# Performance work log

Measured on AMD Instinct MI355X. Metric: run time of the kernel, lower is better.

The kernel has to match this reference:

```python
import jax, jax.numpy as jnp
import numpy as np

NUM_CONTROL_POINTS = 4
# Standard Catmull-Rom spline basis (rows map [1, t, t^2, t^3] monomials to control points)
CATMULL_ROM_BASIS = 0.5 * np.array(
    [[0.0, 2.0, 0.0, 0.0],
     [-1.0, 0.0, 1.0, 0.0],
     [2.0, -5.0, 4.0, -1.0],
     [-1.0, 3.0, -3.0, 1.0]], dtype=np.float32)

BATCH, IN_F, OUT_F = 1024, 512, 512


def setup_inputs() -> dict:
    key = jax.random.key(0)
    k1, k2, k3, k4 = jax.random.split(key, 4)
    inp = jax.random.normal(k1, (BATCH, IN_F), dtype=jnp.float32)
    # phase spans [0, 2*pi) so both spline segments (mask = phase < 1.5*pi) are exercised
    phase = jax.random.uniform(k2, (BATCH,), dtype=jnp.float32) * (2.0 * jnp.pi)
    bound = 1.0 / np.sqrt(IN_F)
    weights = jax.random.uniform(k3, (NUM_CONTROL_POINTS, OUT_F, IN_F), dtype=jnp.float32,
                                 minval=-bound, maxval=bound)
    biases = jax.random.uniform(k4, (NUM_CONTROL_POINTS, OUT_F), dtype=jnp.float32,
                                minval=-bound, maxval=bound)
    return {"input": inp, "phase": phase, "weights": weights, "biases": biases}


def _spline_coeffs(phase):
    # Faithful to the original (including its overwrite bug): tt = [1, t^2, t^3, 0]
    basis = jnp.asarray(CATMULL_ROM_BASIS, dtype=phase.dtype)
    t0 = phase / (1.5 * jnp.pi)
    t1 = (phase - 0.5 * jnp.pi) / (1.5 * jnp.pi)
    ones, zeros = jnp.ones_like(phase), jnp.zeros_like(phase)
    tt0 = jnp.stack([ones, t0 * t0, t0 ** 3, zeros], axis=1)  # (B,4)
    tt1 = jnp.stack([ones, t1 * t1, t1 ** 3, zeros], axis=1)  # (B,4)
    mask = (phase < 1.5 * jnp.pi)[:, None]
    # Selecting per-sample coefficients before the weight contraction is exactly
    # equivalent to where(mask, tt0@B@W, tt1@B@W) since the map is linear in tt.
    return jnp.where(mask, tt0 @ basis, tt1 @ basis)  # (B,4) control-point coeffs


def reference(input, phase, weights, biases):
    c = _spline_coeffs(phase)                       # (B,4)
    # Fused form: apply the 4 shared control-point linear layers, then blend,
    # avoiding the (B,out,in) per-sample weight tensor. Same math as
    # (tt@B@W).reshape(B,out,in) @ input[:,:,None] + b.
    y4 = jnp.einsum('bi,coi->bco', input, weights)  # (B,4,out)
    out = jnp.einsum('bc,bco->bo', c, y4) + c @ biases  # (B,out)
    return out
```

## Files before the change

kernel.cpp:

```cpp
#include <hip/hip_runtime.h>


#define BATCH 1024
#define IN_F  512
#define OUT_F 512

constexpr int BM = 32;
constexpr int BO = 32;
constexpr int BK = 32;
constexpr int KITERS = IN_F / BK;

typedef unsigned short u16;
typedef __bf16 bf16x8 __attribute__((ext_vector_type(8)));
typedef float  f32x4  __attribute__((ext_vector_type(4)));
typedef float  f32x8  __attribute__((ext_vector_type(8)));

__device__ __forceinline__ bf16x8 cvt8(f32x8 v) {
  bf16x8 r;
#pragma unroll
  for (int i = 0; i < 8; ++i) r[i] = (__bf16)v[i];
  return r;
}

__global__ __launch_bounds__(128)
void PhaseLinear_kernel(const float* __restrict__ inp, const float* __restrict__ ph,
                        const float* __restrict__ wts, const float* __restrict__ bia,
                        float* __restrict__ outp) {
  __shared__ float sCoef[BM][4];

  const int tid = threadIdx.x;
  const int wv  = tid >> 6;
  const int l   = tid & 63;
  const int o0  = blockIdx.x * BO;
  const int b0  = blockIdx.y * BM;

  if (tid < BM) {
    const float PI = 3.14159265358979323846f;
    float p  = ph[b0 + tid];
    float t  = (p < 1.5f * PI) ? (p / (1.5f * PI)) : ((p - 0.5f * PI) / (1.5f * PI));
    float t2 = t * t, t3 = t2 * t;
    sCoef[tid][0] = t3 - 0.5f * t2;
    sCoef[tid][1] = 1.0f - 2.5f * t3;
    sCoef[tid][2] = 0.5f * t2 + 2.0f * t3;
    sCoef[tid][3] = -0.5f * t3;
  }
  __syncthreads();

  const int n = l & 15;
  const int q = l >> 4;

  const float* pa0 = inp + (size_t)(b0 + n) * IN_F + q * 8;
  const float* pa1 = pa0 + (size_t)16 * IN_F;
  const float* pw[4];
#pragma unroll
  for (int c = 0; c < 4; ++c)
    pw[c] = wts + ((size_t)c * OUT_F + o0 + wv * 16 + n) * IN_F + q * 8;

  f32x4 acc[2][4];
#pragma unroll
  for (int m = 0; m < 2; ++m)
#pragma unroll
    for (int c = 0; c < 4; ++c) acc[m][c] = (f32x4){0.f, 0.f, 0.f, 0.f};

  f32x8 cur[6];
  cur[0] = *(const f32x8*)(pa0);
  cur[1] = *(const f32x8*)(pa1);
#pragma unroll
  for (int c = 0; c < 4; ++c) cur[2 + c] = *(const f32x8*)(pw[c]);

#pragma unroll
  for (int kk = 0; kk < KITERS; ++kk) {
    f32x8 nxt[6];
    if (kk + 1 < KITERS) {
      const int off = (kk + 1) * BK;
      nxt[0] = *(const f32x8*)(pa0 + off);
      nxt[1] = *(const f32x8*)(pa1 + off);
#pragma unroll
      for (int c = 0; c < 4; ++c) nxt[2 + c] = *(const f32x8*)(pw[c] + off);
    }
    bf16x8 a0 = cvt8(cur[0]);
    bf16x8 a1 = cvt8(cur[1]);
#pragma unroll
    for (int c = 0; c < 4; ++c) {
      bf16x8 wf = cvt8(cur[2 + c]);
      acc[0][c] = __builtin_amdgcn_mfma_f32_16x16x32_bf16(a0, wf, acc[0][c], 0, 0, 0);
      acc[1][c] = __builtin_amdgcn_mfma_f32_16x16x32_bf16(a1, wf, acc[1][c], 0, 0, 0);
    }
#pragma unroll
    for (int j = 0; j < 6; ++j) cur[j] = nxt[j];
  }

  const int o = o0 + wv * 16 + n;
  float bs[4];
#pragma unroll
  for (int c = 0; c < 4; ++c) bs[c] = bia[c * OUT_F + o];

#pragma unroll
  for (int mf = 0; mf < 2; ++mf) {
#pragma unroll
    for (int r = 0; r < 4; ++r) {
      const int bl = mf * 16 + q * 4 + r;
      float v = 0.f;
#pragma unroll
      for (int c = 0; c < 4; ++c)
        v += sCoef[bl][c] * (acc[mf][c][r] + bs[c]);
      outp[(size_t)(b0 + bl) * OUT_F + o] = v;
    }
  }
}

extern "C" void kernel_launch(void* const* d_in, const int* in_sizes, int n_in,
                              void* d_out, int out_size, void* d_ws, size_t ws_size,
                              hipStream_t stream) {
  const float* inp = (const float*)d_in[0];
  const float* ph  = (const float*)d_in[1];
  const float* wts = (const float*)d_in[2];
  const float* bia = (const float*)d_in[3];
  float* outp = (float*)d_out;

  dim3 grid(OUT_F / BO, BATCH / BM);
  PhaseLinear_kernel<<<grid, 128, 0, stream>>>(inp, ph, wts, bia, outp);
}
```

Baseline: 84.39 us.

## Pre-convert inputs and weights to bf16 in workspace, enlarge batch tile to 64

Adds a separate conversion kernel that writes bf16 copies of the input and all four weight matrices into the workspace. The GEMM kernel then loads bf16 fragments directly instead of loading fp32 and converting on every iteration, which halves the bytes per load. Each block now holds four waves covering 64 batch rows, and the k-loop is manually double-buffered two steps at a time. The cost is an extra launch and a full read and write pass over the weights and input on every call.

```diff
diff --git a/kernel.cpp b/kernel.cpp
--- a/kernel.cpp
+++ b/kernel.cpp
@@ -5,31 +5,48 @@
 #define IN_F  512
 #define OUT_F 512
 
-constexpr int BM = 32;
+constexpr int BM = 64;
 constexpr int BO = 32;
 constexpr int BK = 32;
 constexpr int KITERS = IN_F / BK;
 
+constexpr int A_VECS = BATCH * IN_F / 4;
+constexpr int W_VECS = 4 * OUT_F * IN_F / 4;
+constexpr int CVT_VECS = A_VECS + W_VECS;
+constexpr size_t WS_A = 0;
+constexpr size_t WS_W = (size_t)BATCH * IN_F;
+
 typedef unsigned short u16;
+typedef __bf16 bf16x4 __attribute__((ext_vector_type(4)));
 typedef __bf16 bf16x8 __attribute__((ext_vector_type(8)));
 typedef float  f32x4  __attribute__((ext_vector_type(4)));
-typedef float  f32x8  __attribute__((ext_vector_type(8)));
 
-__device__ __forceinline__ bf16x8 cvt8(f32x8 v) {
-  bf16x8 r;
+__global__ __launch_bounds__(256)
+void cvt_kernel(const float* __restrict__ inp, const float* __restrict__ wts,
+                __bf16* __restrict__ ws) {
+  int v = blockIdx.x * 256 + threadIdx.x;
+  if (v >= CVT_VECS) return;
+  const float* src; __bf16* dst;
+  if (v < A_VECS) { src = inp + (size_t)v * 4;            dst = ws + WS_A + (size_t)v * 4; }
+  else { int u = v - A_VECS; src = wts + (size_t)u * 4;   dst = ws + WS_W + (size_t)u * 4; }
+  f32x4 x = *(const f32x4*)src;
+  bf16x4 y;
 #pragma unroll
-  for (int i = 0; i < 8; ++i) r[i] = (__bf16)v[i];
-  return r;
+  for (int i = 0; i < 4; ++i) y[i] = (__bf16)x[i];
+  *(bf16x4*)dst = y;
 }
 
-__global__ __launch_bounds__(128)
-void PhaseLinear_kernel(const float* __restrict__ inp, const float* __restrict__ ph,
-                        const float* __restrict__ wts, const float* __restrict__ bia,
-                        float* __restrict__ outp) {
+struct Frag { bf16x8 a0, a1, w0, w1, w2, w3; };
+
+__global__ __launch_bounds__(256)
+void PhaseLinear_kernel(const __bf16* __restrict__ ws, const float* __restrict__ ph,
+                        const float* __restrict__ bia, float* __restrict__ outp) {
   __shared__ float sCoef[BM][4];
 
   const int tid = threadIdx.x;
   const int wv  = tid >> 6;
+  const int wm  = wv & 1;
+  const int wo  = wv >> 1;
   const int l   = tid & 63;
   const int o0  = blockIdx.x * BO;
   const int b0  = blockIdx.y * BM;
@@ -49,12 +66,24 @@
   const int n = l & 15;
   const int q = l >> 4;
 
-  const float* pa0 = inp + (size_t)(b0 + n) * IN_F + q * 8;
-  const float* pa1 = pa0 + (size_t)16 * IN_F;
-  const float* pw[4];
+  const __bf16* pa0 = ws + WS_A + (size_t)(b0 + wm * 32 + n) * IN_F + q * 8;
+  const __bf16* pa1 = pa0 + (size_t)16 * IN_F;
+  const __bf16* pw[4];
 #pragma unroll
   for (int c = 0; c < 4; ++c)
-    pw[c] = wts + ((size_t)c * OUT_F + o0 + wv * 16 + n) * IN_F + q * 8;
+    pw[c] = ws + WS_W + ((size_t)c * OUT_F + o0 + wo * 16 + n) * IN_F + q * 8;
+
+  auto load6 = [&](int kk) -> Frag {
+    const int off = kk * BK;
+    Frag f;
+    f.a0 = *(const bf16x8*)(pa0 + off);
+    f.a1 = *(const bf16x8*)(pa1 + off);
+    f.w0 = *(const bf16x8*)(pw[0] + off);
+    f.w1 = *(const bf16x8*)(pw[1] + off);
+    f.w2 = *(const bf16x8*)(pw[2] + off);
+    f.w3 = *(const bf16x8*)(pw[3] + off);
+    return f;
+  };
 
   f32x4 acc[2][4];
 #pragma unroll
@@ -62,35 +91,27 @@
 #pragma unroll
     for (int c = 0; c < 4; ++c) acc[m][c] = (f32x4){0.f, 0.f, 0.f, 0.f};
 
-  f32x8 cur[6];
-  cur[0] = *(const f32x8*)(pa0);
-  cur[1] = *(const f32x8*)(pa1);
-#pragma unroll
-  for (int c = 0; c < 4; ++c) cur[2 + c] = *(const f32x8*)(pw[c]);
+  auto mfma6 = [&](const Frag& f) {
+    acc[0][0] = __builtin_amdgcn_mfma_f32_16x16x32_bf16(f.a0, f.w0, acc[0][0], 0, 0, 0);
+    acc[1][0] = __builtin_amdgcn_mfma_f32_16x16x32_bf16(f.a1, f.w0, acc[1][0], 0, 0, 0);
+    acc[0][1] = __builtin_amdgcn_mfma_f32_16x16x32_bf16(f.a0, f.w1, acc[0][1], 0, 0, 0);
+    acc[1][1] = __builtin_amdgcn_mfma_f32_16x16x32_bf16(f.a1, f.w1, acc[1][1], 0, 0, 0);
+    acc[0][2] = __builtin_amdgcn_mfma_f32_16x16x32_bf16(f.a0, f.w2, acc[0][2], 0, 0, 0);
+    acc[1][2] = __builtin_amdgcn_mfma_f32_16x16x32_bf16(f.a1, f.w2, acc[1][2], 0, 0, 0);
+    acc[0][3] = __builtin_amdgcn_mfma_f32_16x16x32_bf16(f.a0, f.w3, acc[0][3], 0, 0, 0);
+    acc[1][3] = __builtin_amdgcn_mfma_f32_16x16x32_bf16(f.a1, f.w3, acc[1][3], 0, 0, 0);
+  };
 
-#pragma unroll
-  for (int kk = 0; kk < KITERS; ++kk) {
-    f32x8 nxt[6];
-    if (kk + 1 < KITERS) {
-      const int off = (kk + 1) * BK;
-      nxt[0] = *(const f32x8*)(pa0 + off);
-      nxt[1] = *(const f32x8*)(pa1 + off);
-#pragma unroll
-      for (int c = 0; c < 4; ++c) nxt[2 + c] = *(const f32x8*)(pw[c] + off);
-    }
-    bf16x8 a0 = cvt8(cur[0]);
-    bf16x8 a1 = cvt8(cur[1]);
-#pragma unroll
-    for (int c = 0; c < 4; ++c) {
-      bf16x8 wf = cvt8(cur[2 + c]);
-      acc[0][c] = __builtin_amdgcn_mfma_f32_16x16x32_bf16(a0, wf, acc[0][c], 0, 0, 0);
-      acc[1][c] = __builtin_amdgcn_mfma_f32_16x16x32_bf16(a1, wf, acc[1][c], 0, 0, 0);
-    }
-#pragma unroll
-    for (int j = 0; j < 6; ++j) cur[j] = nxt[j];
+  Frag cur = load6(0);
+#pragma unroll 1
+  for (int kk = 0; kk < KITERS; kk += 2) {
+    Frag nxt = load6(kk + 1);
+    mfma6(cur);
+    if (kk + 2 < KITERS) cur = load6(kk + 2);
+    mfma6(nxt);
   }
 
-  const int o = o0 + wv * 16 + n;
+  const int o = o0 + wo * 16 + n;
   float bs[4];
 #pragma unroll
   for (int c = 0; c < 4; ++c) bs[c] = bia[c * OUT_F + o];
@@ -99,7 +120,7 @@
   for (int mf = 0; mf < 2; ++mf) {
 #pragma unroll
     for (int r = 0; r < 4; ++r) {
-      const int bl = mf * 16 + q * 4 + r;
+      const int bl = wm * 32 + mf * 16 + q * 4 + r;
       float v = 0.f;
 #pragma unroll
       for (int c = 0; c < 4; ++c)
@@ -117,7 +138,10 @@
   const float* wts = (const float*)d_in[2];
   const float* bia = (const float*)d_in[3];
   float* outp = (float*)d_out;
+  __bf16* ws = (__bf16*)d_ws;
+
+  cvt_kernel<<<(CVT_VECS + 255) / 256, 256, 0, stream>>>(inp, wts, ws);
 
   dim3 grid(OUT_F / BO, BATCH / BM);
-  PhaseLinear_kernel<<<grid, 128, 0, stream>>>(inp, ph, wts, bia, outp);
+  PhaseLinear_kernel<<<grid, 256, 0, stream>>>(ws, ph, bia, outp);
 }
```

Result: faster. 78.19 us (-7.4%).
